# Kernel tuning notes

Measured on AMD Instinct MI355X. Metric: run time of the kernel, lower is better.

Reference implementation:

```python
import jax, jax.numpy as jnp
import numpy as np

CH = 640
XD = 768
NH = 8
HD = 80
INNER = NH * HD
EPS = 1e-6


def setup_inputs() -> dict:
    key = jax.random.key(0)
    ks = jax.random.split(key, 8)
    s = lambda fan: 1.0 / np.sqrt(fan)
    return {
        "hidden_states": jax.random.normal(ks[0], (16, CH, 64, 64), jnp.float32),
        "encoder_hidden_states": jax.random.normal(ks[1], (16, 77, XD), jnp.float32),
        "ln_w": jnp.ones((CH,), jnp.float32),
        "ln_b": jnp.zeros((CH,), jnp.float32),
        "wq": jax.random.normal(ks[2], (CH, INNER), jnp.float32) * s(CH),
        "wk": jax.random.normal(ks[3], (XD, INNER), jnp.float32) * s(XD),
        "wv": jax.random.normal(ks[4], (XD, INNER), jnp.float32) * s(XD),
        "wo": jax.random.normal(ks[5], (INNER, CH), jnp.float32) * s(INNER),
        "bo": jnp.zeros((CH,), jnp.float32),
    }


def reference(hidden_states, encoder_hidden_states, ln_w, ln_b, wq, wk, wv, wo, bo):
    B, C, H, W = hidden_states.shape
    residual = hidden_states
    x = hidden_states.reshape(B, C, H * W).transpose(0, 2, 1)  # [B, S, C]
    # LayerNorm over channels
    mu = jnp.mean(x, axis=-1, keepdims=True)
    var = jnp.mean((x - mu) ** 2, axis=-1, keepdims=True)
    xn = (x - mu) * jax.lax.rsqrt(var + EPS) * ln_w + ln_b
    # projections
    q = xn @ wq                       # [B, S, inner]
    k = encoder_hidden_states @ wk    # [B, T, inner]
    v = encoder_hidden_states @ wv
    S = q.shape[1]
    T = k.shape[1]
    q = q.reshape(B, S, NH, HD)
    k = k.reshape(B, T, NH, HD)
    v = v.reshape(B, T, NH, HD)
    scale = 1.0 / np.sqrt(HD)
    scores = jnp.einsum("bshd,bthd->bhst", q, k) * scale
    attn = jax.nn.softmax(scores, axis=-1)
    out = jnp.einsum("bhst,bthd->bshd", attn, v).reshape(B, S, INNER)
    out = out @ wo + bo               # [B, S, C]
    out = out.transpose(0, 2, 1).reshape(B, C, H, W)
    return out + residual
```

## Files before the change

kernel.cpp:

```cpp
#include <hip/hip_runtime.h>

typedef short bf16x8 __attribute__((ext_vector_type(8)));
typedef short bf16x4 __attribute__((ext_vector_type(4)));
typedef float f32x4 __attribute__((ext_vector_type(4)));

#define MFMA16(a, b, c) __builtin_amdgcn_mfma_f32_16x16x32_bf16(a, b, c, 0, 0, 0)

#if defined(__HIP_DEVICE_COMPILE__)
#define MFMAK16(a, b, c) __builtin_amdgcn_mfma_f32_16x16x16bf16_1k(a, b, c, 0, 0, 0)
#else
#define MFMAK16(a, b, c) (c)
#endif

__device__ __forceinline__ short f2bf(float x) {
  unsigned u = __builtin_bit_cast(unsigned, x);
  u += 0x7fffu + ((u >> 16) & 1u);
  return (short)(u >> 16);
}

__device__ __forceinline__ void gload16(const void* g, void* l) {
  __builtin_amdgcn_global_load_lds((const __attribute__((address_space(1))) void*)g,
                                   (__attribute__((address_space(3))) void*)l, 16, 0, 0);
}

#define BB 16
#define SS 4096
#define CC 640
#define TT 77
#define NHH 8
#define HDD 80
#define DP 96
#define MM (BB * SS)

__global__ __launch_bounds__(256) void k_wt(const float* __restrict__ wq,
                                            const float* __restrict__ wo,
                                            const float* __restrict__ wk,
                                            const float* __restrict__ wv,
                                            short* __restrict__ wqT,
                                            short* __restrict__ woT,
                                            short* __restrict__ wkT,
                                            short* __restrict__ wvT) {
  int z = blockIdx.z;
  const float* src = (z == 0) ? wq : (z == 1) ? wo : (z == 2) ? wk : wv;
  short* dst = (z == 0) ? wqT : (z == 1) ? woT : (z == 2) ? wkT : wvT;
  int R = (z < 2) ? 640 : 768;
  int r0 = blockIdx.y * 64;
  if (r0 >= R) return;
  int o0 = blockIdx.x * 64;
  __shared__ float t[64][65];
  int tx = threadIdx.x & 63, ty = threadIdx.x >> 6;
#pragma unroll
  for (int it = 0; it < 16; ++it) {
    int rr = it * 4 + ty;
    t[tx][rr] = src[(size_t)(r0 + rr) * 640 + o0 + tx];
  }
  __syncthreads();
#pragma unroll
  for (int it = 0; it < 16; ++it) {
    int orow = it * 4 + ty;
    dst[(size_t)(o0 + orow) * R + r0 + tx] = f2bf(t[orow][tx]);
  }
}

__global__ __launch_bounds__(256) void k_enc(const float* __restrict__ enc,
                                             short* __restrict__ encb) {
  int idx = (blockIdx.x * 256 + threadIdx.x) * 8;
  int row = idx / 768;
  bf16x8 o = {};
  if (row < 1232) {
    const float* p = enc + (size_t)row * 768 + (idx % 768);
    float4 a0 = *(const float4*)p;
    float4 a1 = *(const float4*)(p + 4);
    o[0] = f2bf(a0.x); o[1] = f2bf(a0.y); o[2] = f2bf(a0.z); o[3] = f2bf(a0.w);
    o[4] = f2bf(a1.x); o[5] = f2bf(a1.y); o[6] = f2bf(a1.z); o[7] = f2bf(a1.w);
  }
  *(bf16x8*)(encb + idx) = o;
}

__global__ __launch_bounds__(256) void k_kv2(const short* __restrict__ encb,
                                             const short* __restrict__ wkT,
                                             const short* __restrict__ wvT,
                                             short* __restrict__ kb,
                                             short* __restrict__ vb) {
  int n0 = blockIdx.x * 128;
  int m0 = blockIdx.y * 128;
  __shared__ short sA[2 * 128 * 32];
  __shared__ short sB[2 * 128 * 32];
  int w = threadIdx.x >> 6, lane = threadIdx.x & 63;
  int col = lane & 15, quad = lane >> 4;
  int wm = w & 1, wn = w >> 1;
  int ldrow = lane >> 2;
  int ldoff = (lane & 3) * 8;
  bool isV = (n0 >= 640);
  const short* wsrc = isV ? (wvT + (size_t)(n0 - 640) * 768) : (wkT + (size_t)n0 * 768);
  const short* gA0 = encb + (size_t)(m0 + w * 32 + ldrow) * 768 + ldoff;
  const short* gA1 = gA0 + 16 * 768;
  const short* gB0 = wsrc + (size_t)(w * 32 + ldrow) * 768 + ldoff;
  const short* gB1 = gB0 + 16 * 768;
  short* lA0 = sA + (w * 32) * 32;
  short* lA1 = lA0 + 16 * 32;
  short* lB0 = sB + (w * 32) * 32;
  short* lB1 = lB0 + 16 * 32;
  f32x4 acc[4][4] = {};
  gload16(gA0, lA0);
  gload16(gA1, lA1);
  gload16(gB0, lB0);
  gload16(gB1, lB1);
  for (int k0 = 0; k0 < 768; k0 += 32) {
    int cur = ((k0 >> 5) & 1) << 12;
    if (k0 + 32 < 768) {
      int nxt = cur ^ 4096;
      gload16(gA0 + k0 + 32, lA0 + nxt);
      gload16(gA1 + k0 + 32, lA1 + nxt);
      gload16(gB0 + k0 + 32, lB0 + nxt);
      gload16(gB1 + k0 + 32, lB1 + nxt);
      asm volatile("s_waitcnt vmcnt(4)" ::: "memory");
    } else {
      asm volatile("s_waitcnt vmcnt(0)" ::: "memory");
    }
    __builtin_amdgcn_s_barrier();
    bf16x8 a[4], bb[4];
#pragma unroll
    for (int mt = 0; mt < 4; ++mt)
      a[mt] = *(const bf16x8*)(sA + cur + (wm * 64 + mt * 16 + col) * 32 + quad * 8);
#pragma unroll
    for (int nt = 0; nt < 4; ++nt)
      bb[nt] = *(const bf16x8*)(sB + cur + (wn * 64 + nt * 16 + col) * 32 + quad * 8);
    asm volatile("s_waitcnt lgkmcnt(0)" ::: "memory");
    __builtin_amdgcn_sched_barrier(0);
    __builtin_amdgcn_s_barrier();
#pragma unroll
    for (int mt = 0; mt < 4; ++mt)
#pragma unroll
      for (int nt = 0; nt < 4; ++nt)
        acc[mt][nt] = MFMA16(a[mt], bb[nt], acc[mt][nt]);
  }
  float scale = isV ? 1.f : 0.11180339887498949f;
#pragma unroll
  for (int mt = 0; mt < 4; ++mt)
#pragma unroll
    for (int nt = 0; nt < 4; ++nt) {
      int i = n0 + wn * 64 + nt * 16 + col;
      int j = isV ? (i - 640) : i;
      int h = j / 80, d = j % 80;
#pragma unroll
      for (int r = 0; r < 4; ++r) {
        int m = m0 + wm * 64 + mt * 16 + quad * 4 + r;
        if (m >= 1232) continue;
        int b = m / 77;
        int t = m - b * 77;
        float v = acc[mt][nt][r] * scale;
        if (isV)
          vb[(((size_t)(b * NHH + h) * 80 + d) * DP) + t] = f2bf(v);
        else
          kb[(((size_t)(b * NHH + h) * 80 + t) * DP) + d] = f2bf(v);
      }
    }
}

__global__ __launch_bounds__(512) void k_ln(const float* __restrict__ hs,
                                            const float* __restrict__ lnw,
                                            const float* __restrict__ lnb,
                                            short* __restrict__ xn) {
  int b = blockIdx.x >> 6;
  int s0 = (blockIdx.x & 63) * 64;
  int t = threadIdx.x;
  int sq = t & 15, cg = t >> 4;
  int s4 = sq * 4;
  const float* base = hs + (size_t)b * CC * SS + s0;
  f32x4 v[20];
  f32x4 sum = {}, sqs = {};
#pragma unroll
  for (int m = 0; m < 20; ++m) {
    int c = cg + m * 32;
    v[m] = *(const f32x4*)(base + (size_t)c * SS + s4);
    sum += v[m];
    sqs += v[m] * v[m];
  }
  __shared__ f32x4 redS[32][16];
  __shared__ f32x4 redQ[32][16];
  __shared__ float smu[64], srs[64];
  redS[cg][sq] = sum;
  redQ[cg][sq] = sqs;
  __syncthreads();
  if (t < 64) {
    int q = t >> 2, j = t & 3;
    float s = 0.f, qq = 0.f;
#pragma unroll
    for (int g = 0; g < 32; ++g) { s += redS[g][q][j]; qq += redQ[g][q][j]; }
    float mu = s * (1.f / 640.f);
    float var = qq * (1.f / 640.f) - mu * mu;
    smu[t] = mu;
    srs[t] = rsqrtf(var + 1e-6f);
  }
  __syncthreads();
  float mu[4], rs[4];
#pragma unroll
  for (int j = 0; j < 4; ++j) { mu[j] = smu[s4 + j]; rs[j] = srs[s4 + j]; }
  __shared__ short tq[64][80];
  short* xrow = xn + (size_t)(b * SS + s0) * 640;
#pragma unroll
  for (int ch = 0; ch < 10; ++ch) {
    int c0 = ch * 64;
    if (ch) __syncthreads();
#pragma unroll
    for (int h = 0; h < 2; ++h) {
      int m = ch * 2 + h;
      int c = c0 + h * 32 + cg;
      float w = lnw[c], bb = lnb[c];
#pragma unroll
      for (int j = 0; j < 4; ++j)
        tq[s4 + j][h * 32 + cg] = f2bf((v[m][j] - mu[j]) * rs[j] * w + bb);
    }
    __syncthreads();
    {
      int s = t >> 3, g = t & 7;
      uint4 x = *(const uint4*)&tq[s][g * 8];
      *(uint4*)(xrow + (size_t)s * 640 + c0 + g * 8) = x;
    }
  }
}

__global__ __launch_bounds__(256) void k_qa(const short* __restrict__ xn,
                                            const short* __restrict__ wqT,
                                            const short* __restrict__ kb,
                                            const short* __restrict__ vb,
                                            short* __restrict__ qws) {
  int s0 = blockIdx.y * 128;
  int pair = blockIdx.x;
  int b = s0 >> 12;
  int t = threadIdx.x;
  int w = t >> 6, lane = t & 63;
  int col = lane & 15, quad = lane >> 4;
  int wm = w & 1, wh = w >> 1;
  int head = pair * 2 + wh;

  __shared__ short smem[4 * 64 * 104];
  short* lA = smem;
  short* lB = smem + 8192;

  int ldrow = lane >> 2, ldoff = (lane & 3) * 8;
  const short* gA = xn + (size_t)(s0 + w * 32 + ldrow) * 640 + ldoff;
  int browbase = (w < 2) ? w * 48 : 96 + (w - 2) * 32;
  const short* gB = wqT + (size_t)(pair * 160 + browbase + ldrow) * 640 + ldoff;
  short* lAw = lA + (w * 32) * 32;
  short* lBw = lB + browbase * 32;

  f32x4 acc[4][5] = {};
  gload16(gA, lAw);
  gload16(gA + 16 * 640, lAw + 16 * 32);
  if (w < 2) {
    gload16(gB, lBw);
    gload16(gB + 16 * 640, lBw + 16 * 32);
    gload16(gB + 32 * 640, lBw + 32 * 32);
  } else {
    gload16(gB, lBw);
    gload16(gB + 16 * 640, lBw + 16 * 32);
  }
  for (int k0 = 0; k0 < 640; k0 += 32) {
    int coA = (k0 & 32) * 128;
    int coB = (k0 & 32) * 160;
    if (k0 + 32 < 640) {
      int nxA = coA ^ 4096;
      int nxB = coB ^ 5120;
      gload16(gA + k0 + 32, lAw + nxA);
      gload16(gA + 16 * 640 + k0 + 32, lAw + nxA + 16 * 32);
      if (w < 2) {
        gload16(gB + k0 + 32, lBw + nxB);
        gload16(gB + 16 * 640 + k0 + 32, lBw + nxB + 16 * 32);
        gload16(gB + 32 * 640 + k0 + 32, lBw + nxB + 32 * 32);
        asm volatile("s_waitcnt vmcnt(5)" ::: "memory");
      } else {
        gload16(gB + k0 + 32, lBw + nxB);
        gload16(gB + 16 * 640 + k0 + 32, lBw + nxB + 16 * 32);
        asm volatile("s_waitcnt vmcnt(4)" ::: "memory");
      }
    } else {
      asm volatile("s_waitcnt vmcnt(0)" ::: "memory");
    }
    __builtin_amdgcn_s_barrier();
    bf16x8 a[4], bb[5];
#pragma unroll
    for (int mt = 0; mt < 4; ++mt)
      a[mt] = *(const bf16x8*)(lA + coA + (wm * 64 + mt * 16 + col) * 32 + quad * 8);
#pragma unroll
    for (int nt = 0; nt < 5; ++nt)
      bb[nt] = *(const bf16x8*)(lB + coB + (wh * 80 + nt * 16 + col) * 32 + quad * 8);
    asm volatile("s_waitcnt lgkmcnt(0)" ::: "memory");
    __builtin_amdgcn_sched_barrier(0);
    __builtin_amdgcn_s_barrier();
#pragma unroll
    for (int mt = 0; mt < 4; ++mt)
#pragma unroll
      for (int nt = 0; nt < 5; ++nt)
        acc[mt][nt] = MFMA16(a[mt], bb[nt], acc[mt][nt]);
  }

  short* ql = smem + w * 6656;
  {
    uint4 z = {0u, 0u, 0u, 0u};
    *(uint4*)&ql[lane * 104 + 80] = z;
    *(uint4*)&ql[lane * 104 + 88] = z;
  }
#pragma unroll
  for (int mt = 0; mt < 4; ++mt)
#pragma unroll
    for (int nt = 0; nt < 5; ++nt)
#pragma unroll
      for (int r = 0; r < 4; ++r)
        ql[(mt * 16 + quad * 4 + r) * 104 + nt * 16 + col] = f2bf(acc[mt][nt][r]);

  const short* kbase = kb + (size_t)(b * NHH + head) * 80 * DP;
  const short* vbase = vb + (size_t)(b * NHH + head) * 80 * DP;
  int kq = quad * 8;
#pragma unroll 1
  for (int sg = 0; sg < 4; ++sg) {
    f32x4 sc[5] = {};
#pragma unroll
    for (int ks = 0; ks < 3; ++ks) {
      int kk = ks * 32 + kq;
      bf16x8 aq = *(const bf16x8*)&ql[(sg * 16 + col) * 104 + kk];
#pragma unroll
      for (int tt = 0; tt < 5; ++tt) {
        bf16x8 bk = *(const bf16x8*)(kbase + (size_t)(tt * 16 + col) * DP + kk);
        sc[tt] = MFMA16(bk, aq, sc[tt]);
      }
    }
    float mx = -1e30f;
#pragma unroll
    for (int tt = 0; tt < 5; ++tt)
#pragma unroll
      for (int r = 0; r < 4; ++r) {
        float v = sc[tt][r];
        if (tt == 4 && r >= 1 && quad == 3) v = -1e30f;
        sc[tt][r] = v;
        mx = fmaxf(mx, v);
      }
    mx = fmaxf(mx, __shfl_xor(mx, 16));
    mx = fmaxf(mx, __shfl_xor(mx, 32));
    float sum = 0.f;
#pragma unroll
    for (int tt = 0; tt < 5; ++tt)
#pragma unroll
      for (int r = 0; r < 4; ++r) {
        float e = __expf(sc[tt][r] - mx);
        sc[tt][r] = e;
        sum += e;
      }
    sum += __shfl_xor(sum, 16);
    sum += __shfl_xor(sum, 32);
    float rl = 1.f / sum;

    bf16x4 pb[5];
#pragma unroll
    for (int tt = 0; tt < 5; ++tt) {
      pb[tt][0] = f2bf(sc[tt][0] * rl);
      pb[tt][1] = f2bf(sc[tt][1] * rl);
      pb[tt][2] = f2bf(sc[tt][2] * rl);
      pb[tt][3] = f2bf(sc[tt][3] * rl);
    }

    f32x4 av[5] = {};
#pragma unroll
    for (int tt = 0; tt < 5; ++tt) {
#pragma unroll
      for (int dt = 0; dt < 5; ++dt) {
        bf16x4 va = *(const bf16x4*)(vbase + (size_t)(dt * 16 + col) * DP + tt * 16 + quad * 4);
        av[dt] = MFMAK16(va, pb[tt], av[dt]);
      }
    }

    size_t srow = (size_t)(s0 + wm * 64 + sg * 16 + col) * 640 + head * 80;
#pragma unroll
    for (int dt = 0; dt < 5; ++dt) {
      bf16x4 o;
      o[0] = f2bf(av[dt][0]);
      o[1] = f2bf(av[dt][1]);
      o[2] = f2bf(av[dt][2]);
      o[3] = f2bf(av[dt][3]);
      *(bf16x4*)(qws + srow + dt * 16 + quad * 4) = o;
    }
  }
}

__global__ __launch_bounds__(512) void k_o(const short* __restrict__ av,
                                           const short* __restrict__ woT,
                                           const float* __restrict__ bo,
                                           const float* __restrict__ hs,
                                           float* __restrict__ out) {
  int s0 = blockIdx.y * 128;
  int c0 = blockIdx.x * 128;
  __shared__ short sA[2 * 128 * 64];
  __shared__ short sB[2 * 128 * 64];
  int w = threadIdx.x >> 6, lane = threadIdx.x & 63;
  int col = lane & 15, quad = lane >> 4;
  int wm = w & 1, wn = w >> 1;

  int lrow = lane >> 3;
  int ss = (lane & 7) ^ lrow;
  const short* gA = av + (size_t)(s0 + w * 8 + lrow) * 640 + ss * 8;
  const short* gB = woT + (size_t)(c0 + w * 8 + lrow) * 640 + ss * 8;

  auto stage = [&](int kt, int bi) {
#pragma unroll
    for (int r = 0; r < 2; ++r) {
      gload16(gA + (size_t)r * 64 * 640 + kt * 64, sA + bi * 8192 + (r * 64 + w * 8) * 64);
      gload16(gB + (size_t)r * 64 * 640 + kt * 64, sB + bi * 8192 + (r * 64 + w * 8) * 64);
    }
  };

  f32x4 acc[4][2] = {};
  stage(0, 0);
  for (int kt = 0; kt < 10; ++kt) {
    int bi = kt & 1;
    if (kt < 9) {
      stage(kt + 1, bi ^ 1);
      asm volatile("s_waitcnt vmcnt(4)" ::: "memory");
    } else {
      asm volatile("s_waitcnt vmcnt(0)" ::: "memory");
    }
    __builtin_amdgcn_s_barrier();
    bf16x8 a[2][4], bb[2][2];
#pragma unroll
    for (int kh = 0; kh < 2; ++kh) {
      int so = ((kh * 4 + quad) ^ (col & 7)) * 8;
#pragma unroll
      for (int mt = 0; mt < 4; ++mt)
        a[kh][mt] = *(const bf16x8*)(sA + bi * 8192 + (wm * 64 + mt * 16 + col) * 64 + so);
#pragma unroll
      for (int nt = 0; nt < 2; ++nt)
        bb[kh][nt] = *(const bf16x8*)(sB + bi * 8192 + (wn * 32 + nt * 16 + col) * 64 + so);
    }
    asm volatile("s_waitcnt lgkmcnt(0)" ::: "memory");
    __builtin_amdgcn_sched_barrier(0);
    __builtin_amdgcn_s_barrier();
#pragma unroll
    for (int kh = 0; kh < 2; ++kh)
#pragma unroll
      for (int mt = 0; mt < 4; ++mt)
#pragma unroll
        for (int nt = 0; nt < 2; ++nt)
          acc[mt][nt] = MFMA16(a[kh][mt], bb[kh][nt], acc[mt][nt]);
  }
  int b = s0 >> 12;
  int sin = s0 & 4095;
  size_t obase = (size_t)b * CC * SS;
#pragma unroll
  for (int mt = 0; mt < 4; ++mt)
#pragma unroll
    for (int nt = 0; nt < 2; ++nt) {
      int s = sin + wm * 64 + mt * 16 + quad * 4;
      int c = c0 + wn * 32 + nt * 16 + col;
      size_t idx = obase + (size_t)c * SS + s;
      float bc = bo[c];
      float4 h = *(const float4*)(hs + idx);
      float4 o;
      o.x = acc[mt][nt][0] + bc + h.x;
      o.y = acc[mt][nt][1] + bc + h.y;
      o.z = acc[mt][nt][2] + bc + h.z;
      o.w = acc[mt][nt][3] + bc + h.w;
      *(float4*)(out + idx) = o;
    }
}

extern "C" void kernel_launch(void* const* d_in, const int* in_sizes, int n_in,
                              void* d_out, int out_size, void* d_ws, size_t ws_size,
                              hipStream_t stream) {
  const float* hs  = (const float*)d_in[0];
  const float* enc = (const float*)d_in[1];
  const float* lnw = (const float*)d_in[2];
  const float* lnb = (const float*)d_in[3];
  const float* wq  = (const float*)d_in[4];
  const float* wk  = (const float*)d_in[5];
  const float* wv  = (const float*)d_in[6];
  const float* wo  = (const float*)d_in[7];
  const float* bo  = (const float*)d_in[8];
  float* out = (float*)d_out;

  char* ws = (char*)d_ws;
  short* wqT = (short*)(ws + 0);
  short* woT = (short*)(ws + 819200);
  short* kb  = (short*)(ws + 1638400);
  short* vb  = (short*)(ws + 3604480);
  short* xn  = (short*)(ws + 5570560);
  short* q   = (short*)(ws + 89456640);
  short* encb = q;
  short* wkT = (short*)(ws + 89456640 + 1966080);
  short* wvT = (short*)(ws + 89456640 + 2949120);

  (void)hipMemsetAsync(ws + 1638400, 0, 3932160, stream);

  k_wt<<<dim3(10, 12, 4), 256, 0, stream>>>(wq, wo, wk, wv, wqT, woT, wkT, wvT);
  k_enc<<<480, 256, 0, stream>>>(enc, encb);
  k_kv2<<<dim3(10, 10), 256, 0, stream>>>(encb, wkT, wvT, kb, vb);
  k_ln<<<1024, 512, 0, stream>>>(hs, lnw, lnb, xn);
  k_qa<<<dim3(4, 512), 256, 0, stream>>>(xn, wqT, kb, vb, q);
  k_o<<<dim3(5, 512), 512, 0, stream>>>(q, woT, bo, hs, out);
}
```

Measured before the change: 349.7 us.

## Remap blocks per XCD, swizzle LDS tiles, and halve attention staging LDS

Both the fused Q-projection/attention kernel and the output-projection kernel now use a 1D grid. Block indices are remapped so that consecutive blocks on the same XCD share sequence tiles, which should improve L2 reuse of the activations and weights. The Q kernel XOR-swizzles its LDS load and read offsets to cut bank conflicts. It also processes the Q tile in two halves so the per-wave staging buffer shrinks, lowering total LDS use and allowing higher occupancy. The extra index arithmetic and the split loop add some overhead.

```diff
diff --git a/kernel.cpp b/kernel.cpp
--- a/kernel.cpp
+++ b/kernel.cpp
@@ -226,8 +226,11 @@
                                             const short* __restrict__ kb,
                                             const short* __restrict__ vb,
                                             short* __restrict__ qws) {
-  int s0 = blockIdx.y * 128;
-  int pair = blockIdx.x;
+  int f = blockIdx.x;
+  int xcd = f & 7;
+  int i = f >> 3;
+  int s0 = (xcd * 64 + (i >> 2)) * 128;
+  int pair = i & 3;
   int b = s0 >> 12;
   int t = threadIdx.x;
   int w = t >> 6, lane = t & 63;
@@ -235,11 +238,12 @@
   int wm = w & 1, wh = w >> 1;
   int head = pair * 2 + wh;
 
-  __shared__ short smem[4 * 64 * 104];
+  __shared__ short smem[18432];
   short* lA = smem;
   short* lB = smem + 8192;
 
-  int ldrow = lane >> 2, ldoff = (lane & 3) * 8;
+  int ldrow = lane >> 2;
+  int ldoff = ((lane & 3) ^ (ldrow & 3)) * 8;
   const short* gA = xn + (size_t)(s0 + w * 32 + ldrow) * 640 + ldoff;
   int browbase = (w < 2) ? w * 48 : 96 + (w - 2) * 32;
   const short* gB = wqT + (size_t)(pair * 160 + browbase + ldrow) * 640 + ldoff;
@@ -257,6 +261,7 @@
     gload16(gB, lBw);
     gload16(gB + 16 * 640, lBw + 16 * 32);
   }
+  int rsw = (col & 3);
   for (int k0 = 0; k0 < 640; k0 += 32) {
     int coA = (k0 & 32) * 128;
     int coB = (k0 & 32) * 160;
@@ -280,12 +285,13 @@
     }
     __builtin_amdgcn_s_barrier();
     bf16x8 a[4], bb[5];
+    int so = (quad ^ rsw) * 8;
 #pragma unroll
     for (int mt = 0; mt < 4; ++mt)
-      a[mt] = *(const bf16x8*)(lA + coA + (wm * 64 + mt * 16 + col) * 32 + quad * 8);
+      a[mt] = *(const bf16x8*)(lA + coA + (wm * 64 + mt * 16 + col) * 32 + so);
 #pragma unroll
     for (int nt = 0; nt < 5; ++nt)
-      bb[nt] = *(const bf16x8*)(lB + coB + (wh * 80 + nt * 16 + col) * 32 + quad * 8);
+      bb[nt] = *(const bf16x8*)(lB + coB + (wh * 80 + nt * 16 + col) * 32 + so);
     asm volatile("s_waitcnt lgkmcnt(0)" ::: "memory");
     __builtin_amdgcn_sched_barrier(0);
     __builtin_amdgcn_s_barrier();
@@ -296,89 +302,93 @@
         acc[mt][nt] = MFMA16(a[mt], bb[nt], acc[mt][nt]);
   }
 
-  short* ql = smem + w * 6656;
-  {
-    uint4 z = {0u, 0u, 0u, 0u};
-    *(uint4*)&ql[lane * 104 + 80] = z;
-    *(uint4*)&ql[lane * 104 + 88] = z;
-  }
-#pragma unroll
-  for (int mt = 0; mt < 4; ++mt)
-#pragma unroll
-    for (int nt = 0; nt < 5; ++nt)
-#pragma unroll
-      for (int r = 0; r < 4; ++r)
-        ql[(mt * 16 + quad * 4 + r) * 104 + nt * 16 + col] = f2bf(acc[mt][nt][r]);
-
+  short* ql = smem + w * 3328;
   const short* kbase = kb + (size_t)(b * NHH + head) * 80 * DP;
   const short* vbase = vb + (size_t)(b * NHH + head) * 80 * DP;
   int kq = quad * 8;
+#pragma unroll
+  for (int h2 = 0; h2 < 2; ++h2) {
+    if (lane < 32) {
+      uint4 z = {0u, 0u, 0u, 0u};
+      *(uint4*)&ql[lane * 104 + 80] = z;
+      *(uint4*)&ql[lane * 104 + 88] = z;
+    }
+#pragma unroll
+    for (int j = 0; j < 2; ++j) {
+      int mt = h2 * 2 + j;
+#pragma unroll
+      for (int nt = 0; nt < 5; ++nt)
+#pragma unroll
+        for (int r = 0; r < 4; ++r)
+          ql[(j * 16 + quad * 4 + r) * 104 + nt * 16 + col] = f2bf(acc[mt][nt][r]);
+    }
 #pragma unroll 1
-  for (int sg = 0; sg < 4; ++sg) {
-    f32x4 sc[5] = {};
-#pragma unroll
-    for (int ks = 0; ks < 3; ++ks) {
-      int kk = ks * 32 + kq;
-      bf16x8 aq = *(const bf16x8*)&ql[(sg * 16 + col) * 104 + kk];
+    for (int sg = 0; sg < 2; ++sg) {
+      f32x4 sc[5] = {};
+#pragma unroll
+      for (int ks = 0; ks < 3; ++ks) {
+        int kk = ks * 32 + kq;
+        bf16x8 aq = *(const bf16x8*)&ql[(sg * 16 + col) * 104 + kk];
+#pragma unroll
+        for (int tt = 0; tt < 5; ++tt) {
+          bf16x8 bk = *(const bf16x8*)(kbase + (size_t)(tt * 16 + col) * DP + kk);
+          sc[tt] = MFMA16(bk, aq, sc[tt]);
+        }
+      }
+      float mx = -1e30f;
+#pragma unroll
+      for (int tt = 0; tt < 5; ++tt)
+#pragma unroll
+        for (int r = 0; r < 4; ++r) {
+          float v = sc[tt][r];
+          if (tt == 4 && r >= 1 && quad == 3) v = -1e30f;
+          sc[tt][r] = v;
+          mx = fmaxf(mx, v);
+        }
+      mx = fmaxf(mx, __shfl_xor(mx, 16));
+      mx = fmaxf(mx, __shfl_xor(mx, 32));
+      float sum = 0.f;
+#pragma unroll
+      for (int tt = 0; tt < 5; ++tt)
+#pragma unroll
+        for (int r = 0; r < 4; ++r) {
+          float e = __expf(sc[tt][r] - mx);
+          sc[tt][r] = e;
+          sum += e;
+        }
+      sum += __shfl_xor(sum, 16);
+      sum += __shfl_xor(sum, 32);
+      float rl = 1.f / sum;
+
+      bf16x4 pb[5];
 #pragma unroll
       for (int tt = 0; tt < 5; ++tt) {
-        bf16x8 bk = *(const bf16x8*)(kbase + (size_t)(tt * 16 + col) * DP + kk);
-        sc[tt] = MFMA16(bk, aq, sc[tt]);
+        pb[tt][0] = f2bf(sc[tt][0] * rl);
+        pb[tt][1] = f2bf(sc[tt][1] * rl);
+        pb[tt][2] = f2bf(sc[tt][2] * rl);
+        pb[tt][3] = f2bf(sc[tt][3] * rl);
       }
-    }
-    float mx = -1e30f;
-#pragma unroll
-    for (int tt = 0; tt < 5; ++tt)
-#pragma unroll
-      for (int r = 0; r < 4; ++r) {
-        float v = sc[tt][r];
-        if (tt == 4 && r >= 1 && quad == 3) v = -1e30f;
-        sc[tt][r] = v;
-        mx = fmaxf(mx, v);
+
+      f32x4 av[5] = {};
+#pragma unroll
+      for (int tt = 0; tt < 5; ++tt) {
+#pragma unroll
+        for (int dt = 0; dt < 5; ++dt) {
+          bf16x4 va = *(const bf16x4*)(vbase + (size_t)(dt * 16 + col) * DP + tt * 16 + quad * 4);
+          av[dt] = MFMAK16(va, pb[tt], av[dt]);
+        }
       }
-    mx = fmaxf(mx, __shfl_xor(mx, 16));
-    mx = fmaxf(mx, __shfl_xor(mx, 32));
-    float sum = 0.f;
-#pragma unroll
-    for (int tt = 0; tt < 5; ++tt)
-#pragma unroll
-      for (int r = 0; r < 4; ++r) {
-        float e = __expf(sc[tt][r] - mx);
-        sc[tt][r] = e;
-        sum += e;
+
+      size_t srow = (size_t)(s0 + wm * 64 + h2 * 32 + sg * 16 + col) * 640 + head * 80;
+#pragma unroll
+      for (int dt = 0; dt < 5; ++dt) {
+        bf16x4 o;
+        o[0] = f2bf(av[dt][0]);
+        o[1] = f2bf(av[dt][1]);
+        o[2] = f2bf(av[dt][2]);
+        o[3] = f2bf(av[dt][3]);
+        *(bf16x4*)(qws + srow + dt * 16 + quad * 4) = o;
       }
-    sum += __shfl_xor(sum, 16);
-    sum += __shfl_xor(sum, 32);
-    float rl = 1.f / sum;
-
-    bf16x4 pb[5];
-#pragma unroll
-    for (int tt = 0; tt < 5; ++tt) {
-      pb[tt][0] = f2bf(sc[tt][0] * rl);
-      pb[tt][1] = f2bf(sc[tt][1] * rl);
-      pb[tt][2] = f2bf(sc[tt][2] * rl);
-      pb[tt][3] = f2bf(sc[tt][3] * rl);
-    }
-
-    f32x4 av[5] = {};
-#pragma unroll
-    for (int tt = 0; tt < 5; ++tt) {
-#pragma unroll
-      for (int dt = 0; dt < 5; ++dt) {
-        bf16x4 va = *(const bf16x4*)(vbase + (size_t)(dt * 16 + col) * DP + tt * 16 + quad * 4);
-        av[dt] = MFMAK16(va, pb[tt], av[dt]);
-      }
-    }
-
-    size_t srow = (size_t)(s0 + wm * 64 + sg * 16 + col) * 640 + head * 80;
-#pragma unroll
-    for (int dt = 0; dt < 5; ++dt) {
-      bf16x4 o;
-      o[0] = f2bf(av[dt][0]);
-      o[1] = f2bf(av[dt][1]);
-      o[2] = f2bf(av[dt][2]);
-      o[3] = f2bf(av[dt][3]);
-      *(bf16x4*)(qws + srow + dt * 16 + quad * 4) = o;
     }
   }
 }
@@ -388,8 +398,13 @@
                                            const float* __restrict__ bo,
                                            const float* __restrict__ hs,
                                            float* __restrict__ out) {
-  int s0 = blockIdx.y * 128;
-  int c0 = blockIdx.x * 128;
+  int f = blockIdx.x;
+  int xcd = f & 7;
+  int i = f >> 3;
+  int st = xcd * 64 + i / 5;
+  int ct = i - (i / 5) * 5;
+  int s0 = st * 128;
+  int c0 = ct * 128;
   __shared__ short sA[2 * 128 * 64];
   __shared__ short sB[2 * 128 * 64];
   int w = threadIdx.x >> 6, lane = threadIdx.x & 63;
@@ -494,6 +509,6 @@
   k_enc<<<480, 256, 0, stream>>>(enc, encb);
   k_kv2<<<dim3(10, 10), 256, 0, stream>>>(encb, wkT, wvT, kb, vb);
   k_ln<<<1024, 512, 0, stream>>>(hs, lnw, lnb, xn);
-  k_qa<<<dim3(4, 512), 256, 0, stream>>>(xn, wqT, kb, vb, q);
-  k_o<<<dim3(5, 512), 512, 0, stream>>>(q, woT, bo, hs, out);
-}
+  k_qa<<<2048, 256, 0, stream>>>(xn, wqT, kb, vb, q);
+  k_o<<<2560, 512, 0, stream>>>(q, woT, bo, hs, out);
+}
```

Measured after the change: 380.9 us. 8.9% more time.
